# Kernel optimization log

Hardware: AMD Instinct MI355X
Metric: run time of the kernel (lower is better)

Reference implementation:

```python
import jax, jax.numpy as jnp
import numpy as np
from jax import lax

# ---- static config (ProposalLayer config object) ----
BASE_SIZE = 16
RATIOS = np.array([0.5, 1.0, 2.0])
SCALES = np.array([8.0, 16.0, 32.0])
STRIDE = 16
PRE_NMS_TOPN = 6000
POST_NMS_TOPN = 300
MIN_THRESHOLD = 16.0
NMS_THRESH = 0.7
IMG_W = 4096
IMG_H = 2048
NEG_INF = jnp.float32(-1e30)


def _generate_anchors(base_size, ratios, scales):
    w = h = float(base_size)
    x_ctr = y_ctr = 0.5 * (base_size - 1)
    size = w * h
    size_ratios = size / ratios
    ws = np.round(np.sqrt(size_ratios))          # (R,)
    hs = np.round(ws * ratios)                   # (R,)
    ws = (ws[:, None] * scales[None, :]).ravel() # (R*S,)
    hs = (hs[:, None] * scales[None, :]).ravel()
    anchors = np.stack([x_ctr - 0.5 * (ws - 1), y_ctr - 0.5 * (hs - 1),
                        x_ctr + 0.5 * (ws - 1), y_ctr + 0.5 * (hs - 1)], axis=1)
    return anchors.astype(np.float32)            # (A, 4) in x1,y1,x2,y2


def _all_anchors(height, width, stride):
    anchors = _generate_anchors(BASE_SIZE, RATIOS, SCALES)      # (A,4)
    sx = np.arange(width) * stride
    sy = np.arange(height) * stride
    mx, my = np.meshgrid(sx, sy)                                # (H,W) each
    shifts = np.stack([mx.ravel(), my.ravel(), mx.ravel(), my.ravel()], axis=1)
    shifts = shifts.reshape(-1, 1, 4).astype(np.float32)        # (K,1,4), K iterates h-major
    return (anchors[None] + shifts).reshape(-1, 4)              # (K*A, 4)


def _decode(deltas, anchors):
    # deltas: (B, N, 4); anchors: (N, 4) -> boxes (B, N, 4)
    aw = anchors[:, 2] - anchors[:, 0] + 1.0
    ah = anchors[:, 3] - anchors[:, 1] + 1.0
    acx = anchors[:, 0] + 0.5 * (aw - 1.0)
    acy = anchors[:, 1] + 0.5 * (ah - 1.0)
    dx, dy, dw, dh = deltas[..., 0], deltas[..., 1], deltas[..., 2], deltas[..., 3]
    pcx = dx * aw + acx
    pcy = dy * ah + acy
    pw = jnp.exp(dw) * aw
    ph = jnp.exp(dh) * ah
    return jnp.stack([pcx - 0.5 * pw, pcy - 0.5 * ph,
                      pcx + 0.5 * pw, pcy + 0.5 * ph], axis=-1)


def _nms_single(boxes, scores):
    # boxes (N,4), scores (N,) -> greedy NMS, fixed POST_NMS_TOPN outputs
    areas = (boxes[:, 2] - boxes[:, 0] + 1.0) * (boxes[:, 3] - boxes[:, 1] + 1.0)

    def body(live, _):
        i = jnp.argmax(live)
        box = boxes[i]
        sc = scores[i]
        xx1 = jnp.maximum(box[0], boxes[:, 0])
        yy1 = jnp.maximum(box[1], boxes[:, 1])
        xx2 = jnp.minimum(box[2], boxes[:, 2])
        yy2 = jnp.minimum(box[3], boxes[:, 3])
        inter = jnp.maximum(xx2 - xx1 + 1.0, 0.0) * jnp.maximum(yy2 - yy1 + 1.0, 0.0)
        iou = inter / (areas[i] + areas - inter)
        live = jnp.where(iou > NMS_THRESH, NEG_INF, live)
        live = live.at[i].set(NEG_INF)
        return live, (box, sc)

    _, (out_boxes, out_scores) = lax.scan(body, scores, None, length=POST_NMS_TOPN)
    return out_boxes, out_scores  # (P,4), (P,)


def reference(labels_pred, bbox_reg):
    B = labels_pred.shape[0]
    H, W = labels_pred.shape[-2:]
    anchors = jnp.asarray(_all_anchors(H, W, STRIDE))           # (K*A,4)

    # objectness score = fg channel after (B,2A,H,W)->(B,H,W,2A)->(B,KA,2)
    scores = jnp.transpose(labels_pred, (0, 2, 3, 1)).reshape(B, -1, 2)[..., 1]
    deltas = jnp.transpose(bbox_reg, (0, 2, 3, 1)).reshape(B, -1, 4)

    boxes = _decode(deltas, anchors)                            # (B,KA,4)
    x = jnp.clip(boxes[..., 0::2], 0.0, IMG_W - 1.0)
    y = jnp.clip(boxes[..., 1::2], 0.0, IMG_H - 1.0)
    boxes = jnp.stack([x[..., 0], y[..., 0], x[..., 1], y[..., 1]], axis=-1)

    keep = ((boxes[..., 2] - boxes[..., 0] + 1.0 >= MIN_THRESHOLD) &
            (boxes[..., 3] - boxes[..., 1] + 1.0 >= MIN_THRESHOLD))
    masked = jnp.where(keep, scores, NEG_INF)

    # pre-NMS top-k of kept anchors by score (assumes keep.sum >= PRE_NMS_TOPN)
    top_scores_masked, idx = lax.top_k(masked, PRE_NMS_TOPN)    # (B,P)
    top_scores = jnp.take_along_axis(scores, idx, axis=1)
    top_boxes = jnp.take_along_axis(boxes, idx[..., None], axis=1)

    out_boxes, out_scores = jax.vmap(_nms_single)(top_boxes, top_scores)
    return out_boxes, out_scores


def setup_inputs() -> dict:
    key = jax.random.key(0)
    k1, k2 = jax.random.split(key)
    labels_pred = jax.random.normal(k1, (16, 18, 128, 256), dtype=jnp.float32)
    bbox_reg = jax.random.normal(k2, (16, 36, 128, 256), dtype=jnp.float32)
    return {"labels_pred": labels_pred, "bbox_reg": bbox_reg}
```

## Files before the change

### kernel.cpp

```cpp
#include <hip/hip_runtime.h>
#include <stdint.h>

#define NBATCH 16
#define NANCH  9
#define NHGT   128
#define NWID   256
#define NHW    (NHGT * NWID)
#define NTOT   (NHW * NANCH)
#define PRE    6000
#define POST   300
#define CAPN   8192
#define BINS   8192
#define BIN_SHIFT 19
#define NWORDS 94
#define RROWS  384
#define SWORDS 6

#define MIDP 0x1.6666668p-1

__device__ __constant__ float c_AW[NANCH] = {184.f,368.f,736.f,128.f,256.f,512.f,88.f,176.f,352.f};
__device__ __constant__ float c_AH[NANCH] = {96.f,192.f,384.f,128.f,256.f,512.f,176.f,352.f,704.f};

__device__ __forceinline__ uint32_t f2key(float f) {
    uint32_t u = __float_as_uint(f);
    return (u & 0x80000000u) ? ~u : (u | 0x80000000u);
}

__device__ __forceinline__ bool iou_sup(const float4 bi, float areaI, const float4 bj, float areaJ) {
    float xx1 = fmaxf(bi.x, bj.x);
    float yy1 = fmaxf(bi.y, bj.y);
    float xx2 = fminf(bi.z, bj.z);
    float yy2 = fminf(bi.w, bj.w);
    float iw = fmaxf(__fadd_rn(__fsub_rn(xx2, xx1), 1.f), 0.f);
    float ih = fmaxf(__fadd_rn(__fsub_rn(yy2, yy1), 1.f), 0.f);
    float inter = __fmul_rn(iw, ih);
    float uni = __fsub_rn(__fadd_rn(areaI, areaJ), inter);
    return ((double)inter >= (double)uni * MIDP);
}

__device__ __forceinline__ bool decode_clip(float dx, float dy, float dw, float dh,
                                            float aw, float ah, float acx, float acy,
                                            float& x1, float& y1, float& x2, float& y2) {
    float pcx = __fadd_rn(__fmul_rn(dx, aw), acx);
    float pcy = __fadd_rn(__fmul_rn(dy, ah), acy);
    float pw  = __fmul_rn(expf(dw), aw);
    float ph  = __fmul_rn(expf(dh), ah);
    float hx  = __fmul_rn(0.5f, pw);
    float hy  = __fmul_rn(0.5f, ph);
    x1 = __fsub_rn(pcx, hx);
    y1 = __fsub_rn(pcy, hy);
    x2 = __fadd_rn(pcx, hx);
    y2 = __fadd_rn(pcy, hy);
    x1 = fminf(fmaxf(x1, 0.f), 4095.f);
    x2 = fminf(fmaxf(x2, 0.f), 4095.f);
    y1 = fminf(fmaxf(y1, 0.f), 2047.f);
    y2 = fminf(fmaxf(y2, 0.f), 2047.f);
    float wpl = __fadd_rn(__fsub_rn(x2, x1), 1.f);
    float hpl = __fadd_rn(__fsub_rn(y2, y1), 1.f);
    return (wpl >= 16.f) && (hpl >= 16.f);
}

__global__ __launch_bounds__(256) void k_zero(uint4* __restrict__ ghist4,
                                              uint32_t* __restrict__ cntthr) {
    int g = blockIdx.x * 256 + threadIdx.x;
    if (blockIdx.x < 128) {
        ghist4[g] = make_uint4(0, 0, 0, 0);
    } else {
        if (threadIdx.x < 32) cntthr[threadIdx.x] = 0;
    }
}

__global__ __launch_bounds__(256) void k_hist(const float* __restrict__ lab,
                                              const float* __restrict__ reg,
                                              uint32_t* __restrict__ ghist,
                                              uint32_t* __restrict__ keys) {
    __shared__ uint32_t hist[BINS];
    for (int i = threadIdx.x; i < BINS; i += 256) hist[i] = 0;
    __syncthreads();
    int b = blockIdx.x >> 5, sub = blockIdx.x & 31;
    int hw = (sub << 10) | (threadIdx.x << 2);
    int h = hw >> 8, w = hw & 255;
    const float* lb = lab + (size_t)b * 18 * NHW + hw;
    const float* rb = reg + (size_t)b * 36 * NHW + hw;
    uint32_t* kb = keys + (size_t)b * NANCH * NHW + hw;
    float acy  = (float)(h * 16) + 7.5f;
    float acx0 = (float)(w * 16) + 7.5f;
    float acx1 = acx0 + 16.0f;
    float acx2 = acx0 + 32.0f;
    float acx3 = acx0 + 48.0f;
#pragma unroll
    for (int a = 0; a < NANCH; ++a) {
        float4 s  = *(const float4*)&lb[(2 * a + 1) * NHW];
        float4 dx = *(const float4*)&rb[(4 * a + 0) * NHW];
        float4 dy = *(const float4*)&rb[(4 * a + 1) * NHW];
        float4 dwv = *(const float4*)&rb[(4 * a + 2) * NHW];
        float4 dhv = *(const float4*)&rb[(4 * a + 3) * NHW];
        float x1, y1, x2, y2;
        bool k0 = decode_clip(dx.x, dy.x, dwv.x, dhv.x, c_AW[a], c_AH[a], acx0, acy, x1, y1, x2, y2);
        bool k1 = decode_clip(dx.y, dy.y, dwv.y, dhv.y, c_AW[a], c_AH[a], acx1, acy, x1, y1, x2, y2);
        bool k2 = decode_clip(dx.z, dy.z, dwv.z, dhv.z, c_AW[a], c_AH[a], acx2, acy, x1, y1, x2, y2);
        bool k3 = decode_clip(dx.w, dy.w, dwv.w, dhv.w, c_AW[a], c_AH[a], acx3, acy, x1, y1, x2, y2);
        uint32_t key0 = f2key(k0 ? s.x : -1e30f);
        uint32_t key1 = f2key(k1 ? s.y : -1e30f);
        uint32_t key2 = f2key(k2 ? s.z : -1e30f);
        uint32_t key3 = f2key(k3 ? s.w : -1e30f);
        *(uint4*)&kb[a * NHW] = make_uint4(key0, key1, key2, key3);
        atomicAdd(&hist[key0 >> BIN_SHIFT], 1u);
        atomicAdd(&hist[key1 >> BIN_SHIFT], 1u);
        atomicAdd(&hist[key2 >> BIN_SHIFT], 1u);
        atomicAdd(&hist[key3 >> BIN_SHIFT], 1u);
    }
    __syncthreads();
    uint32_t* gh = ghist + ((size_t)b << 13);
    for (int i = threadIdx.x; i < BINS; i += 256) {
        uint32_t c = hist[i];
        if (c) atomicAdd(&gh[i], c);
    }
}

__global__ __launch_bounds__(256) void k_thresh(const uint32_t* __restrict__ ghist,
                                                uint32_t* __restrict__ thresh) {
    __shared__ uint32_t part[256];
    int b = blockIdx.x;
    const uint32_t* gh = ghist + ((size_t)b << 13);
    uint32_t p = 0;
    int base = threadIdx.x * 32;
    for (int k = 0; k < 32; ++k) p += gh[base + k];
    part[threadIdx.x] = p;
    __syncthreads();
    if (threadIdx.x == 0) {
        uint32_t cum = 0;
        int tb = 0;
        for (int c = 255; c >= 0; --c) {
            if (cum + part[c] >= (uint32_t)PRE) {
                for (int i = 31; i >= 0; --i) {
                    cum += gh[c * 32 + i];
                    if (cum >= (uint32_t)PRE) { tb = c * 32 + i; break; }
                }
                break;
            }
            cum += part[c];
        }
        thresh[b] = (uint32_t)tb << BIN_SHIFT;
    }
}

__global__ __launch_bounds__(256) void k_compact(const uint32_t* __restrict__ keys,
                                                 const uint32_t* __restrict__ thresh,
                                                 uint32_t* __restrict__ cnt,
                                                 uint64_t* __restrict__ cand) {
    __shared__ uint64_t stage[2304];
    __shared__ uint32_t sCount;
    __shared__ uint32_t sBase;
    if (threadIdx.x == 0) sCount = 0;
    __syncthreads();
    int bid = blockIdx.x;
    int b = bid >> 7;
    int hw = ((bid & 127) << 8) | threadIdx.x;
    int lane = threadIdx.x & 63;
    const uint32_t* kb = keys + (size_t)b * NANCH * NHW + hw;
    uint32_t th = thresh[b];
#pragma unroll
    for (int a = 0; a < NANCH; ++a) {
        uint32_t key = kb[a * NHW];
        bool valid = (key >= th);
        uint64_t mask = __ballot(valid);
        if (mask) {
            int leader = __ffsll((unsigned long long)mask) - 1;
            uint32_t wb = 0;
            if (lane == leader) wb = atomicAdd(&sCount, (uint32_t)__popcll(mask));
            wb = (uint32_t)__shfl((int)wb, leader);
            if (valid) {
                int rank = __popcll(mask & ((1ull << lane) - 1ull));
                uint32_t n = (uint32_t)(hw * NANCH + a);
                stage[wb + rank] = ((uint64_t)key << 32) | (uint32_t)(~n);
            }
        }
    }
    __syncthreads();
    if (threadIdx.x == 0) sBase = atomicAdd(&cnt[b], sCount);
    __syncthreads();
    uint32_t total = sCount, base = sBase;
    for (uint32_t i = threadIdx.x; i < total; i += 256) {
        uint32_t pos = base + i;
        if (pos < (uint32_t)CAPN) cand[(size_t)b * CAPN + pos] = stage[i];
    }
}

__global__ __launch_bounds__(512) void k_sortA(const uint32_t* __restrict__ cnt,
                                               uint64_t* __restrict__ cand) {
    __shared__ uint64_t sm[1024];
    int b = blockIdx.x >> 3, c = blockIdx.x & 7;
    uint32_t C = cnt[b];
    if (C > (uint32_t)CAPN) C = CAPN;
    uint64_t* cb = cand + (size_t)b * CAPN;
    int base = c << 10;
    for (int li = threadIdx.x; li < 1024; li += 512) {
        int gi = base + li;
        sm[li] = (gi < (int)C) ? cb[gi] : 0ull;
    }
    __syncthreads();
    for (int k = 2; k <= 1024; k <<= 1) {
        for (int j = k >> 1; j > 0; j >>= 1) {
            for (int li = threadIdx.x; li < 1024; li += 512) {
                int lxj = li ^ j;
                if (lxj > li) {
                    uint64_t va = sm[li], vb = sm[lxj];
                    bool up = ((li & k) == 0);
                    bool sw = up ? (va < vb) : (va > vb);
                    if (sw) { sm[li] = vb; sm[lxj] = va; }
                }
            }
            __syncthreads();
        }
    }
    for (int li = threadIdx.x; li < 1024; li += 512) cb[base + li] = sm[li];
}

__global__ __launch_bounds__(256) void k_merge(const uint64_t* __restrict__ src,
                                               uint64_t* __restrict__ dst,
                                               int Rlog) {
    int g = blockIdx.x * 256 + threadIdx.x;
    if (g >= NBATCH * CAPN) return;
    int b = g >> 13;
    int p = g & (CAPN - 1);
    int R = 1 << Rlog;
    int pair = p >> (Rlog + 1);
    int q = p & ((R << 1) - 1);
    const uint64_t* A = src + (size_t)b * CAPN + ((size_t)(pair << 1) << Rlog);
    const uint64_t* B = A + R;
    int lo = (q > R) ? (q - R) : 0;
    int hi = (q < R) ? q : R;
    while (lo < hi) {
        int mid = (lo + hi) >> 1;
        if (A[mid] > B[q - mid - 1]) lo = mid + 1; else hi = mid;
    }
    int i = lo, j = q - lo;
    uint64_t aV = (i < R) ? A[i] : 0ull;
    uint64_t bV = (j < R) ? B[j] : 0ull;
    dst[(size_t)b * CAPN + p] = (aV > bV) ? aV : bV;
}

__global__ __launch_bounds__(256) void k_mergegather(const uint64_t* __restrict__ cand,
                                                     const float* __restrict__ lab,
                                                     const float* __restrict__ reg,
                                                     float4* __restrict__ boxes,
                                                     float* __restrict__ scores) {
    int g = blockIdx.x * 256 + threadIdx.x;
    if (g >= NBATCH * PRE) return;
    int b = g / PRE, p = g - b * PRE;
    const uint64_t* A = cand + (size_t)b * CAPN;
    const uint64_t* B = A + 4096;
    int lo = (p > 4096) ? (p - 4096) : 0;
    int hi = (p < 4096) ? p : 4096;
    while (lo < hi) {
        int mid = (lo + hi) >> 1;
        if (A[mid] > B[p - mid - 1]) lo = mid + 1; else hi = mid;
    }
    int i = lo, j = p - lo;
    uint64_t aV = (i < 4096) ? A[i] : 0ull;
    uint64_t bV = (j < 4096) ? B[j] : 0ull;
    uint64_t v = (aV > bV) ? aV : bV;
    uint32_t n = ~(uint32_t)(v & 0xFFFFFFFFull);
    if (n >= (uint32_t)NTOT) n = 0;
    int a = (int)(n % NANCH);
    int hw = (int)(n / NANCH);
    int w = hw & 255, h = hw >> 8;
    const float* lb0 = lab + (size_t)b * 18 * NHW;
    const float* rb0 = reg + (size_t)b * 36 * NHW;
    float s  = lb0[(2 * a + 1) * NHW + hw];
    float dx = rb0[(4 * a + 0) * NHW + hw];
    float dy = rb0[(4 * a + 1) * NHW + hw];
    float dwv = rb0[(4 * a + 2) * NHW + hw];
    float dhv = rb0[(4 * a + 3) * NHW + hw];
    float acx = (float)(w * 16) + 7.5f;
    float acy = (float)(h * 16) + 7.5f;
    float x1, y1, x2, y2;
    decode_clip(dx, dy, dwv, dhv, c_AW[a], c_AH[a], acx, acy, x1, y1, x2, y2);
    boxes[b * PRE + p] = make_float4(x1, y1, x2, y2);
    scores[b * PRE + p] = s;
}

__global__ __launch_bounds__(512) void k_iou(const float4* __restrict__ boxes,
                                             uint64_t* __restrict__ supp) {
    __shared__ float4 lb[RROWS];
    __shared__ float  la[RROWS];
    int blk = blockIdx.x % 48;
    int b   = blockIdx.x / 48;
    const float4* bb = boxes + b * PRE;
    for (int i = threadIdx.x; i < RROWS; i += 512) {
        float4 v = bb[i];
        lb[i] = v;
        la[i] = __fmul_rn(__fadd_rn(__fsub_rn(v.z, v.x), 1.f),
                          __fadd_rn(__fsub_rn(v.w, v.y), 1.f));
    }
    __syncthreads();
    int wave = threadIdx.x >> 6, lane = threadIdx.x & 63;
    int r = (blk << 3) + wave;
    float4 bi = lb[r];
    float ai = la[r];
    uint64_t* sr = supp + ((size_t)b * RROWS + r) * SWORDS;
#pragma unroll
    for (int w = 0; w < SWORDS; ++w) {
        int j = (w << 6) | lane;
        bool s = iou_sup(bi, ai, lb[j], la[j]);
        uint64_t m = __ballot(s);
        if (lane == 0) sr[w] = m;
    }
}

#define RD32(V, L) __builtin_amdgcn_readlane((uint32_t)(V), (L))
#define RDL64(V, L) ((uint64_t)(uint32_t)RD32((V), (L)) | \
                     ((uint64_t)(uint32_t)RD32((uint32_t)((V) >> 32), (L)) << 32))

#define LOADW(I) do {                                                           \
    const uint64_t* _rp = sbase + (size_t)(((I) << 6) + lane) * SWORDS;         \
    m##I##0 = _rp[0]; m##I##1 = _rp[1]; m##I##2 = _rp[2];                       \
    m##I##3 = _rp[3]; m##I##4 = _rp[4]; m##I##5 = _rp[5];                       \
} while (0)

#define WINDOW(I) {                                                             \
    uint64_t curw = s##I;                                                       \
    while (curw) {                                                              \
        int rl = __ffsll((unsigned long long)curw) - 1;                         \
        if (lane == 0) idxb[t] = (uint32_t)(((I) << 6) + rl);                   \
        ++t;                                                                    \
        s0 &= ~RDL64(m##I##0, rl); s1 &= ~RDL64(m##I##1, rl);                   \
        s2 &= ~RDL64(m##I##2, rl); s3 &= ~RDL64(m##I##3, rl);                   \
        s4 &= ~RDL64(m##I##4, rl); s5 &= ~RDL64(m##I##5, rl);                   \
        if (t >= POST) { flag = 0; goto walk_done; }                            \
        curw = s##I;                                                            \
    }                                                                           \
}

__global__ __launch_bounds__(64, 1) void k_walk(const uint64_t* __restrict__ supp,
                                                uint32_t* __restrict__ flags,
                                                uint32_t* __restrict__ idxAll) {
    int b = blockIdx.x;
    int lane = threadIdx.x;
    uint32_t* idxb = idxAll + b * POST;
    const uint64_t* sbase = supp + (size_t)b * RROWS * SWORDS;
    uint64_t m00,m01,m02,m03,m04,m05;
    uint64_t m10,m11,m12,m13,m14,m15;
    uint64_t m20,m21,m22,m23,m24,m25;
    uint64_t m30,m31,m32,m33,m34,m35;
    uint64_t m40,m41,m42,m43,m44,m45;
    uint64_t m50,m51,m52,m53,m54,m55;
    LOADW(0); LOADW(1); LOADW(2); LOADW(3); LOADW(4); LOADW(5);
    uint64_t s0 = ~0ull, s1 = ~0ull, s2 = ~0ull, s3 = ~0ull, s4 = ~0ull, s5 = ~0ull;
    int t = 0;
    int flag = 1;
    WINDOW(0)
    WINDOW(1)
    WINDOW(2)
    WINDOW(3)
    WINDOW(4)
    WINDOW(5)
walk_done:
    if (lane == 0) flags[b] = (uint32_t)flag;
}

__global__ __launch_bounds__(512) void k_resume(const float4* __restrict__ boxes,
                                                const uint32_t* __restrict__ flags,
                                                uint32_t* __restrict__ idxAll) {
    int b = blockIdx.x;
    if (flags[b] == 0) return;
    __shared__ uint64_t alive[NWORDS];
    __shared__ uint32_t sCur;
    int tid = threadIdx.x;
    const float4* bb = boxes + b * PRE;
    uint32_t* idxb = idxAll + b * POST;
    if (tid < NWORDS) alive[tid] = (tid == NWORDS - 1) ? ((1ull << 48) - 1ull) : ~0ull;
    __syncthreads();
    for (int t = 0; t < POST; ++t) {
        if (tid == 0) sCur = 0xFFFFFFFFu;
        __syncthreads();
        if (tid < NWORDS) {
            uint64_t wd = alive[tid];
            if (wd) atomicMin(&sCur, (uint32_t)(tid * 64 + (__ffsll((unsigned long long)wd) - 1)));
        }
        __syncthreads();
        uint32_t cur = sCur;
        uint32_t e = (cur < (uint32_t)PRE) ? cur : 0u;
        if (tid == 0) {
            idxb[t] = e;
            if (cur < (uint32_t)PRE)
                atomicAnd(&alive[cur >> 6], ~(1ull << (cur & 63)));
        }
        if (cur < (uint32_t)PRE) {
            float4 bc = bb[e];
            float areaC = __fmul_rn(__fadd_rn(__fsub_rn(bc.z, bc.x), 1.f),
                                    __fadd_rn(__fsub_rn(bc.w, bc.y), 1.f));
            for (uint32_t j = cur + 1 + tid; j < (uint32_t)PRE; j += 512) {
                uint64_t wd = alive[j >> 6];
                if ((wd >> (j & 63)) & 1ull) {
                    float4 bj = bb[j];
                    float areaJ = __fmul_rn(__fadd_rn(__fsub_rn(bj.z, bj.x), 1.f),
                                            __fadd_rn(__fsub_rn(bj.w, bj.y), 1.f));
                    if (iou_sup(bc, areaC, bj, areaJ))
                        atomicAnd(&alive[j >> 6], ~(1ull << (j & 63)));
                }
            }
        }
        __syncthreads();
    }
}

__global__ __launch_bounds__(256) void k_out(const float4* __restrict__ boxes,
                                             const float* __restrict__ scores,
                                             const uint32_t* __restrict__ idxAll,
                                             float* __restrict__ out) {
    int g = blockIdx.x * 256 + threadIdx.x;
    if (g >= NBATCH * POST) return;
    int b = g / POST;
    uint32_t i = idxAll[g];
    if (i >= (uint32_t)PRE) i = 0;
    float4 bc = boxes[b * PRE + i];
    size_t ob = (size_t)g * 4;
    out[ob + 0] = bc.x; out[ob + 1] = bc.y;
    out[ob + 2] = bc.z; out[ob + 3] = bc.w;
    out[(size_t)NBATCH * POST * 4 + g] = scores[b * PRE + i];
}

extern "C" void kernel_launch(void* const* d_in, const int* in_sizes, int n_in,
                              void* d_out, int out_size, void* d_ws, size_t ws_size,
                              hipStream_t stream) {
    (void)in_sizes; (void)n_in; (void)out_size; (void)ws_size;
    const float* lab = (const float*)d_in[0];
    const float* reg = (const float*)d_in[1];
    float* out = (float*)d_out;
    char* ws = (char*)d_ws;

    uint32_t* ghist  = (uint32_t*)(ws + 0);
    uint32_t* cnt    = (uint32_t*)(ws + 524288);
    uint32_t* thr    = (uint32_t*)(ws + 524352);
    uint64_t* cand   = (uint64_t*)(ws + 524416);
    float4*   boxes  = (float4*)  (ws + 1572992);
    float*    scores = (float*)   (ws + 3108992);
    uint64_t* supp   = (uint64_t*)(ws + 3492992);
    uint32_t* flags  = (uint32_t*)(ws + 3787904);
    uint32_t* idx    = (uint32_t*)(ws + 3787968);
    uint32_t* keys   = (uint32_t*)(ws + 3807168);
    uint64_t* cand2  = (uint64_t*)(ws + 22681536);

    k_zero       <<<129, 256, 0, stream>>>((uint4*)ghist, cnt);
    k_hist       <<<512, 256, 0, stream>>>(lab, reg, ghist, keys);
    k_thresh     <<<NBATCH, 256, 0, stream>>>(ghist, thr);
    k_compact    <<<2048, 256, 0, stream>>>(keys, thr, cnt, cand);
    k_sortA      <<<NBATCH * 8, 512, 0, stream>>>(cnt, cand);
    k_merge      <<<NBATCH * CAPN / 256, 256, 0, stream>>>(cand, cand2, 10);
    k_merge      <<<NBATCH * CAPN / 256, 256, 0, stream>>>(cand2, cand, 11);
    k_mergegather<<<(NBATCH * PRE + 255) / 256, 256, 0, stream>>>(cand, lab, reg, boxes, scores);
    k_iou        <<<NBATCH * 48, 512, 0, stream>>>(boxes, supp);
    k_walk       <<<NBATCH, 64, 0, stream>>>(supp, flags, idx);
    k_resume     <<<NBATCH, 512, 0, stream>>>(boxes, flags, idx);
    k_out        <<<(NBATCH * POST + 255) / 256, 256, 0, stream>>>(boxes, scores, idx, out);
}
```

Before: 152.7 us.

## Fuse merge passes into one LDS kernel and fold output writes into NMS

```diff
diff --git a/kernel.cpp b/kernel.cpp
--- a/kernel.cpp
+++ b/kernel.cpp
@@ -60,14 +60,8 @@
     return (wpl >= 16.f) && (hpl >= 16.f);
 }
 
-__global__ __launch_bounds__(256) void k_zero(uint4* __restrict__ ghist4,
-                                              uint32_t* __restrict__ cntthr) {
-    int g = blockIdx.x * 256 + threadIdx.x;
-    if (blockIdx.x < 128) {
-        ghist4[g] = make_uint4(0, 0, 0, 0);
-    } else {
-        if (threadIdx.x < 32) cntthr[threadIdx.x] = 0;
-    }
+__global__ __launch_bounds__(256) void k_zero(uint4* __restrict__ ghist4) {
+    ghist4[blockIdx.x * 256 + threadIdx.x] = make_uint4(0, 0, 0, 0);
 }
 
 __global__ __launch_bounds__(256) void k_hist(const float* __restrict__ lab,
@@ -119,7 +113,8 @@
 }
 
 __global__ __launch_bounds__(256) void k_thresh(const uint32_t* __restrict__ ghist,
-                                                uint32_t* __restrict__ thresh) {
+                                                uint32_t* __restrict__ thresh,
+                                                uint32_t* __restrict__ cnt) {
     __shared__ uint32_t part[256];
     int b = blockIdx.x;
     const uint32_t* gh = ghist + ((size_t)b << 13);
@@ -142,6 +137,7 @@
             cum += part[c];
         }
         thresh[b] = (uint32_t)tb << BIN_SHIFT;
+        cnt[b] = 0;
     }
 }
 
@@ -217,17 +213,11 @@
     for (int li = threadIdx.x; li < 1024; li += 512) cb[base + li] = sm[li];
 }
 
-__global__ __launch_bounds__(256) void k_merge(const uint64_t* __restrict__ src,
-                                               uint64_t* __restrict__ dst,
-                                               int Rlog) {
-    int g = blockIdx.x * 256 + threadIdx.x;
-    if (g >= NBATCH * CAPN) return;
-    int b = g >> 13;
-    int p = g & (CAPN - 1);
+__device__ __forceinline__ uint64_t mp_elem(const uint64_t* __restrict__ sm, int p, int Rlog) {
     int R = 1 << Rlog;
     int pair = p >> (Rlog + 1);
     int q = p & ((R << 1) - 1);
-    const uint64_t* A = src + (size_t)b * CAPN + ((size_t)(pair << 1) << Rlog);
+    const uint64_t* A = sm + ((size_t)(pair << 1) << Rlog);
     const uint64_t* B = A + R;
     int lo = (q > R) ? (q - R) : 0;
     int hi = (q < R) ? q : R;
@@ -238,29 +228,48 @@
     int i = lo, j = q - lo;
     uint64_t aV = (i < R) ? A[i] : 0ull;
     uint64_t bV = (j < R) ? B[j] : 0ull;
-    dst[(size_t)b * CAPN + p] = (aV > bV) ? aV : bV;
-}
-
-__global__ __launch_bounds__(256) void k_mergegather(const uint64_t* __restrict__ cand,
-                                                     const float* __restrict__ lab,
-                                                     const float* __restrict__ reg,
-                                                     float4* __restrict__ boxes,
-                                                     float* __restrict__ scores) {
+    return (aV > bV) ? aV : bV;
+}
+
+__global__ __launch_bounds__(1024) void k_merge2(uint64_t* __restrict__ cand) {
+    __shared__ uint64_t sm[CAPN];
+    int b = blockIdx.x;
+    uint64_t* cb = cand + (size_t)b * CAPN;
+    for (int i = threadIdx.x; i < CAPN; i += 1024) sm[i] = cb[i];
+    __syncthreads();
+#pragma unroll
+    for (int lvl = 10; lvl <= 12; ++lvl) {
+        uint64_t v0 = mp_elem(sm, threadIdx.x + 0 * 1024, lvl);
+        uint64_t v1 = mp_elem(sm, threadIdx.x + 1 * 1024, lvl);
+        uint64_t v2 = mp_elem(sm, threadIdx.x + 2 * 1024, lvl);
+        uint64_t v3 = mp_elem(sm, threadIdx.x + 3 * 1024, lvl);
+        uint64_t v4 = mp_elem(sm, threadIdx.x + 4 * 1024, lvl);
+        uint64_t v5 = mp_elem(sm, threadIdx.x + 5 * 1024, lvl);
+        uint64_t v6 = mp_elem(sm, threadIdx.x + 6 * 1024, lvl);
+        uint64_t v7 = mp_elem(sm, threadIdx.x + 7 * 1024, lvl);
+        __syncthreads();
+        sm[threadIdx.x + 0 * 1024] = v0;
+        sm[threadIdx.x + 1 * 1024] = v1;
+        sm[threadIdx.x + 2 * 1024] = v2;
+        sm[threadIdx.x + 3 * 1024] = v3;
+        sm[threadIdx.x + 4 * 1024] = v4;
+        sm[threadIdx.x + 5 * 1024] = v5;
+        sm[threadIdx.x + 6 * 1024] = v6;
+        sm[threadIdx.x + 7 * 1024] = v7;
+        __syncthreads();
+    }
+    for (int i = threadIdx.x; i < CAPN; i += 1024) cb[i] = sm[i];
+}
+
+__global__ __launch_bounds__(256) void k_gather(const uint64_t* __restrict__ cand,
+                                                const float* __restrict__ lab,
+                                                const float* __restrict__ reg,
+                                                float4* __restrict__ boxes,
+                                                float* __restrict__ scores) {
     int g = blockIdx.x * 256 + threadIdx.x;
     if (g >= NBATCH * PRE) return;
     int b = g / PRE, p = g - b * PRE;
-    const uint64_t* A = cand + (size_t)b * CAPN;
-    const uint64_t* B = A + 4096;
-    int lo = (p > 4096) ? (p - 4096) : 0;
-    int hi = (p < 4096) ? p : 4096;
-    while (lo < hi) {
-        int mid = (lo + hi) >> 1;
-        if (A[mid] > B[p - mid - 1]) lo = mid + 1; else hi = mid;
-    }
-    int i = lo, j = p - lo;
-    uint64_t aV = (i < 4096) ? A[i] : 0ull;
-    uint64_t bV = (j < 4096) ? B[j] : 0ull;
-    uint64_t v = (aV > bV) ? aV : bV;
+    uint64_t v = cand[(size_t)b * CAPN + p];
     uint32_t n = ~(uint32_t)(v & 0xFFFFFFFFull);
     if (n >= (uint32_t)NTOT) n = 0;
     int a = (int)(n % NANCH);
@@ -323,22 +332,24 @@
     uint64_t curw = s##I;                                                       \
     while (curw) {                                                              \
         int rl = __ffsll((unsigned long long)curw) - 1;                         \
-        if (lane == 0) idxb[t] = (uint32_t)(((I) << 6) + rl);                   \
+        if (lane == 0) sidx[t] = (uint32_t)(((I) << 6) + rl);                   \
         ++t;                                                                    \
         s0 &= ~RDL64(m##I##0, rl); s1 &= ~RDL64(m##I##1, rl);                   \
         s2 &= ~RDL64(m##I##2, rl); s3 &= ~RDL64(m##I##3, rl);                   \
         s4 &= ~RDL64(m##I##4, rl); s5 &= ~RDL64(m##I##5, rl);                   \
-        if (t >= POST) { flag = 0; goto walk_done; }                            \
+        if (t >= POST) goto walk_done;                                          \
         curw = s##I;                                                            \
     }                                                                           \
 }
 
 __global__ __launch_bounds__(64, 1) void k_walk(const uint64_t* __restrict__ supp,
+                                                const float4* __restrict__ boxes,
+                                                const float* __restrict__ scores,
                                                 uint32_t* __restrict__ flags,
-                                                uint32_t* __restrict__ idxAll) {
+                                                float* __restrict__ out) {
+    __shared__ uint32_t sidx[POST];
     int b = blockIdx.x;
     int lane = threadIdx.x;
-    uint32_t* idxb = idxAll + b * POST;
     const uint64_t* sbase = supp + (size_t)b * RROWS * SWORDS;
     uint64_t m00,m01,m02,m03,m04,m05;
     uint64_t m10,m11,m12,m13,m14,m15;
@@ -349,27 +360,38 @@
     LOADW(0); LOADW(1); LOADW(2); LOADW(3); LOADW(4); LOADW(5);
     uint64_t s0 = ~0ull, s1 = ~0ull, s2 = ~0ull, s3 = ~0ull, s4 = ~0ull, s5 = ~0ull;
     int t = 0;
-    int flag = 1;
     WINDOW(0)
     WINDOW(1)
     WINDOW(2)
     WINDOW(3)
     WINDOW(4)
     WINDOW(5)
+    if (lane == 0) flags[b] = 1u;
+    return;
 walk_done:
-    if (lane == 0) flags[b] = (uint32_t)flag;
+    __syncthreads();
+    for (int tt = lane; tt < POST; tt += 64) {
+        uint32_t i = sidx[tt];
+        float4 bc = boxes[b * PRE + i];
+        size_t ob = ((size_t)b * POST + tt) * 4;
+        out[ob + 0] = bc.x; out[ob + 1] = bc.y;
+        out[ob + 2] = bc.z; out[ob + 3] = bc.w;
+        out[(size_t)NBATCH * POST * 4 + (size_t)b * POST + tt] = scores[b * PRE + i];
+    }
+    if (lane == 0) flags[b] = 0u;
 }
 
 __global__ __launch_bounds__(512) void k_resume(const float4* __restrict__ boxes,
+                                                const float* __restrict__ scores,
                                                 const uint32_t* __restrict__ flags,
-                                                uint32_t* __restrict__ idxAll) {
+                                                float* __restrict__ out) {
     int b = blockIdx.x;
     if (flags[b] == 0) return;
     __shared__ uint64_t alive[NWORDS];
     __shared__ uint32_t sCur;
     int tid = threadIdx.x;
     const float4* bb = boxes + b * PRE;
-    uint32_t* idxb = idxAll + b * POST;
+    const float* sb = scores + b * PRE;
     if (tid < NWORDS) alive[tid] = (tid == NWORDS - 1) ? ((1ull << 48) - 1ull) : ~0ull;
     __syncthreads();
     for (int t = 0; t < POST; ++t) {
@@ -382,13 +404,16 @@
         __syncthreads();
         uint32_t cur = sCur;
         uint32_t e = (cur < (uint32_t)PRE) ? cur : 0u;
+        float4 bc = bb[e];
         if (tid == 0) {
-            idxb[t] = e;
+            size_t ob = ((size_t)b * POST + t) * 4;
+            out[ob + 0] = bc.x; out[ob + 1] = bc.y;
+            out[ob + 2] = bc.z; out[ob + 3] = bc.w;
+            out[(size_t)NBATCH * POST * 4 + (size_t)b * POST + t] = sb[e];
             if (cur < (uint32_t)PRE)
                 atomicAnd(&alive[cur >> 6], ~(1ull << (cur & 63)));
         }
         if (cur < (uint32_t)PRE) {
-            float4 bc = bb[e];
             float areaC = __fmul_rn(__fadd_rn(__fsub_rn(bc.z, bc.x), 1.f),
                                     __fadd_rn(__fsub_rn(bc.w, bc.y), 1.f));
             for (uint32_t j = cur + 1 + tid; j < (uint32_t)PRE; j += 512) {
@@ -406,22 +431,6 @@
     }
 }
 
-__global__ __launch_bounds__(256) void k_out(const float4* __restrict__ boxes,
-                                             const float* __restrict__ scores,
-                                             const uint32_t* __restrict__ idxAll,
-                                             float* __restrict__ out) {
-    int g = blockIdx.x * 256 + threadIdx.x;
-    if (g >= NBATCH * POST) return;
-    int b = g / POST;
-    uint32_t i = idxAll[g];
-    if (i >= (uint32_t)PRE) i = 0;
-    float4 bc = boxes[b * PRE + i];
-    size_t ob = (size_t)g * 4;
-    out[ob + 0] = bc.x; out[ob + 1] = bc.y;
-    out[ob + 2] = bc.z; out[ob + 3] = bc.w;
-    out[(size_t)NBATCH * POST * 4 + g] = scores[b * PRE + i];
-}
-
 extern "C" void kernel_launch(void* const* d_in, const int* in_sizes, int n_in,
                               void* d_out, int out_size, void* d_ws, size_t ws_size,
                               hipStream_t stream) {
@@ -439,20 +448,16 @@
     float*    scores = (float*)   (ws + 3108992);
     uint64_t* supp   = (uint64_t*)(ws + 3492992);
     uint32_t* flags  = (uint32_t*)(ws + 3787904);
-    uint32_t* idx    = (uint32_t*)(ws + 3787968);
-    uint32_t* keys   = (uint32_t*)(ws + 3807168);
-    uint64_t* cand2  = (uint64_t*)(ws + 22681536);
-
-    k_zero       <<<129, 256, 0, stream>>>((uint4*)ghist, cnt);
-    k_hist       <<<512, 256, 0, stream>>>(lab, reg, ghist, keys);
-    k_thresh     <<<NBATCH, 256, 0, stream>>>(ghist, thr);
-    k_compact    <<<2048, 256, 0, stream>>>(keys, thr, cnt, cand);
-    k_sortA      <<<NBATCH * 8, 512, 0, stream>>>(cnt, cand);
-    k_merge      <<<NBATCH * CAPN / 256, 256, 0, stream>>>(cand, cand2, 10);
-    k_merge      <<<NBATCH * CAPN / 256, 256, 0, stream>>>(cand2, cand, 11);
-    k_mergegather<<<(NBATCH * PRE + 255) / 256, 256, 0, stream>>>(cand, lab, reg, boxes, scores);
-    k_iou        <<<NBATCH * 48, 512, 0, stream>>>(boxes, supp);
-    k_walk       <<<NBATCH, 64, 0, stream>>>(supp, flags, idx);
-    k_resume     <<<NBATCH, 512, 0, stream>>>(boxes, flags, idx);
-    k_out        <<<(NBATCH * POST + 255) / 256, 256, 0, stream>>>(boxes, scores, idx, out);
-}
+    uint32_t* keys   = (uint32_t*)(ws + 3787968);
+
+    k_zero   <<<128, 256, 0, stream>>>((uint4*)ghist);
+    k_hist   <<<512, 256, 0, stream>>>(lab, reg, ghist, keys);
+    k_thresh <<<NBATCH, 256, 0, stream>>>(ghist, thr, cnt);
+    k_compact<<<2048, 256, 0, stream>>>(keys, thr, cnt, cand);
+    k_sortA  <<<NBATCH * 8, 512, 0, stream>>>(cnt, cand);
+    k_merge2 <<<NBATCH, 1024, 0, stream>>>(cand);
+    k_gather <<<(NBATCH * PRE + 255) / 256, 256, 0, stream>>>(cand, lab, reg, boxes, scores);
+    k_iou    <<<NBATCH * 48, 512, 0, stream>>>(boxes, supp);
+    k_walk   <<<NBATCH, 64, 0, stream>>>(supp, boxes, scores, flags, out);
+    k_resume <<<NBATCH, 512, 0, stream>>>(boxes, scores, flags, out);
+}
```

After: 165.3 us. 8.3% more time.
